# Performance work log

Measured on AMD Instinct MI355X. Metric: run time of the kernel, lower is better.

Reference implementation:

```python
import jax, jax.numpy as jnp
import numpy as np

FFT_LIST = [32, 64, 128]
C_IN = 64
C_OUT = 96
C_OUT_PER = C_OUT // len(FFT_LIST)  # 32
BASIC = FFT_LIST[1]                 # base kernel defined at fft=64 -> 33 bins
ALPHA = 0.2                         # tf.nn.leaky_relu default


def setup_inputs() -> dict:
    key = jax.random.key(0)
    k1, k2, k3, k4 = jax.random.split(key, 4)
    B, T = 8, 8192
    bins0 = BASIC // 2 + 1
    return {
        "x": jax.random.normal(k1, (B, T, C_IN), dtype=jnp.float32),
        "kernel_r": jax.random.normal(k2, (1, 1, bins0, C_IN * C_OUT_PER), dtype=jnp.float32) * 0.05,
        "kernel_i": jax.random.normal(k3, (1, 1, bins0, C_IN * C_OUT_PER), dtype=jnp.float32) * 0.05,
        "bias_r": jax.random.normal(k4, (C_OUT,), dtype=jnp.float32) * 0.05,
    }


def _resize_bins(k, bins):
    # tf.image.resize on [1, H=1, W=bins0, C]: bilinear along W, half-pixel, no antialias
    if bins == k.shape[2]:
        return k
    return jax.image.resize(k, (1, 1, bins, k.shape[3]), method="linear", antialias=False)


def _leaky(v):
    return jax.nn.leaky_relu(v, negative_slope=ALPHA)


def reference(x, kernel_r, kernel_i, bias_r):
    B, T, _ = x.shape
    xc = jnp.transpose(x, (0, 2, 1))  # [B, C_in, T]
    outs = []
    for fft_n in FFT_LIST:
        frames = T // fft_n
        bins = fft_n // 2 + 1
        # non-overlapping STFT with no window == reshape + rfft
        xf = jnp.fft.rfft(xc.reshape(B, C_IN, frames, fft_n), axis=-1)  # [B, Cin, F, K] complex64
        kr = _resize_bins(kernel_r, bins)
        ki = _resize_bins(kernel_i, bins)
        kern = (kr + 1j * ki).reshape(bins, C_IN, C_OUT_PER).astype(jnp.complex64)  # [K, Cin, Cout]
        # per-frequency-bin complex matmul over c_in (fuses tile+mul+reduce_sum)
        y = jnp.einsum("bcfk,kco->bofk", xf, kern)  # [B, Cout, F, K]
        # act_domain == 'freq': leaky relu on real and imag parts
        y = _leaky(jnp.real(y)) + 1j * _leaky(jnp.imag(y))
        # inverse STFT (step == length, no window) == irfft + reshape
        yt = jnp.fft.irfft(y, n=fft_n, axis=-1)            # [B, Cout, F, fft_n]
        yt = yt.reshape(B, C_OUT_PER, T)                    # [B, Cout, T]
        outs.append(jnp.transpose(yt, (0, 2, 1)))           # [B, T, Cout]
    out = jnp.concatenate(outs, axis=2)                     # [B, T, C_OUT]
    out = out + bias_r                                      # bias_add(real(bias))
    return out
```

## Files before the change

kernel.cpp:

```cpp
#include <hip/hip_runtime.h>
#include <stdint.h>

#define T_SZ 8192
#define NCH 96

typedef __attribute__((ext_vector_type(8))) short s8v;
typedef __attribute__((ext_vector_type(4))) float f4v;

__device__ __forceinline__ float lo_bf(uint32_t u){ return __uint_as_float(u << 16); }
__device__ __forceinline__ float hi_bf(uint32_t u){ return __uint_as_float(u & 0xffff0000u); }
__device__ __forceinline__ uint32_t f2bf(float f){
    uint32_t u = __float_as_uint(f);
    return (u + 0x7fffu + ((u >> 16) & 1u)) >> 16;
}
__device__ __forceinline__ uint32_t pk2(float a, float b){ return f2bf(a) | (f2bf(b) << 16); }

#define WS_TOTAL_PAIRS 235520
#define WD_OFF    942080
#define WD_ELEMS  27264
#define WA_OFF    996608
#define WA_ELEMS  30464
#define WD64_U16   1920
#define WD128_U16  7680
#define WA64_U16   2304
#define WA128_U16  8960
#define XF32W    4194304
#define XF64W   14680064
#define XF128W  25165824
#define Y32W    35651584
#define Y64W    41943040
#define Y128W   50331648
#define WS_WIDE 58720256

__global__ void prep_full(char* __restrict__ ws)
{
    int e = blockIdx.x * 256 + threadIdx.x;
    if (e < WD_ELEMS) {
        int N, NP, base;
        if (e < 1920)      { N = 32;  NP = 40;  base = 0; }
        else if (e < 7680) { N = 64;  NP = 72;  base = WD64_U16;  e -= 1920; }
        else               { N = 128; NP = 136; base = WD128_U16; e -= 7680; }
        int m = e / NP, t = e % NP;
        float v = 0.f;
        if (t < N && m < N + 2) {
            float ang = 6.2831853071795864769f * (float)(((m >> 1) * t) & (N - 1)) / (float)N;
            v = (m & 1) ? -sinf(ang) : cosf(ang);
        }
        ((unsigned short*)(ws + WD_OFF))[base + e] = (unsigned short)f2bf(v);
        return;
    }
    e -= WD_ELEMS;
    if (e < WA_ELEMS) {
        int N, S3, base;
        if (e < 2304)      { N = 32;  S3 = 72;  base = 0; }
        else if (e < 8960) { N = 64;  S3 = 104; base = WA64_U16;  e -= 2304; }
        else               { N = 128; S3 = 168; base = WA128_U16; e -= 8960; }
        int t = e / S3, kk = e % S3;
        int M2 = N + 2;
        float v = 0.f;
        if (kk < M2) {
            int k = kk >> 1;
            float ang = 6.2831853071795864769f * (float)((k * t) & (N - 1)) / (float)N;
            v = (kk & 1) ? -sinf(ang) : cosf(ang);
        }
        ((unsigned short*)(ws + WA_OFF))[base + e] = (unsigned short)f2bf(v);
    }
}

__global__ void prep_resize(const float* __restrict__ kr, const float* __restrict__ ki,
                            uint32_t* __restrict__ wsu)
{
    int idx = blockIdx.x * 256 + threadIdx.x;
    if (idx >= WS_TOTAL_PAIRS) return;
    int bins, rem = idx;
    if (rem < 17 * 2048)      { bins = 17; }
    else if (rem < 50 * 2048) { bins = 33; rem -= 17 * 2048; }
    else                      { bins = 65; rem -= 50 * 2048; }
    int k = rem >> 11, co = rem & 2047;
    float s  = (k + 0.5f) * (33.0f / bins) - 0.5f;
    float fl = floorf(s);
    float w1 = s - fl;
    int i0 = min(max((int)fl, 0), 32);
    int i1 = min(max((int)fl + 1, 0), 32);
    float r0 = kr[i0 * 2048 + co], r1 = kr[i1 * 2048 + co];
    float q0 = ki[i0 * 2048 + co], q1 = ki[i1 * 2048 + co];
    wsu[idx] = pk2(fmaf(w1, r1 - r0, r0), fmaf(w1, q1 - q0, q0));
}

__device__ __forceinline__ s8v ldfr(const unsigned short* p, int stride, int row0, int k0){
    int lane = threadIdx.x & 63;
    return *(const s8v*)(p + (row0 + (lane & 15)) * stride + k0 + ((lane >> 4) << 3));
}

template<int N, int NTW, int MT0, int MTN>
__device__ __forceinline__ void k1w_branch(const unsigned short* __restrict__ W,
        const unsigned short* __restrict__ xT, uint32_t* __restrict__ xfp,
        int b, int w, int nt0)
{
    constexpr int BINS = N/2+1, KS = N/32, NP = N+8;
    constexpr int F = 128/N, FRAMES = 8192/N;
    const int lane = threadIdx.x & 63;
    const int cl = lane & 15, kl = (lane >> 4) << 3, rg = (lane >> 4) * 4;

    f4v acc[MTN][NTW];
    #pragma unroll
    for (int mt = 0; mt < MTN; ++mt)
        #pragma unroll
        for (int nw = 0; nw < NTW; ++nw) { f4v zz = {0.f,0.f,0.f,0.f}; acc[mt][nw] = zz; }

    for (int ks = 0; ks < KS; ++ks) {
        s8v a[MTN];
        #pragma unroll
        for (int mt = 0; mt < MTN; ++mt) a[mt] = ldfr(W, NP, (MT0+mt)*16, ks*32);
        #pragma unroll
        for (int nw = 0; nw < NTW; ++nw) {
            int rowb = (nt0+nw)*16 + cl;
            s8v bb = *(const s8v*)(xT + (rowb & 63)*136 + (rowb >> 6)*N + ks*32 + kl);
            #pragma unroll
            for (int mt = 0; mt < MTN; ++mt)
                acc[mt][nw] = __builtin_amdgcn_mfma_f32_16x16x32_bf16(a[mt], bb, acc[mt][nw], 0, 0, 0);
        }
    }
    #pragma unroll
    for (int mt = 0; mt < MTN; ++mt)
      #pragma unroll
      for (int nw = 0; nw < NTW; ++nw) {
        int col = (nt0+nw)*16 + cl, f = col >> 6, c = col & 63;
        size_t bf = (size_t)b*FRAMES + w*F + f;
        #pragma unroll
        for (int r = 0; r < 4; r += 2) {
            int m = (MT0+mt)*16 + rg + r, k = m >> 1;
            if (k < BINS)
                xfp[((size_t)k*(8*FRAMES) + bf)*64 + c] = pk2(acc[mt][nw][r], acc[mt][nw][r+1]);
        }
      }
}

__global__ __launch_bounds__(512, 4) void k1w(const float* __restrict__ x, char* __restrict__ ws)
{
    __shared__ __align__(16) char smem[71936];
    unsigned short* xT   = (unsigned short*)smem;
    unsigned short* Wall = xT + 64*136;
    const unsigned short* WD = (const unsigned short*)(ws + WD_OFF);
    const int tid = threadIdx.x, bid = blockIdx.x;
    const int b = bid >> 6, w = bid & 63;

    for (int e = tid; e < WD_ELEMS/8; e += 512)
        *(uint4*)(Wall + e*8) = *(const uint4*)(WD + e*8);

    const float* xb = x + ((size_t)b*T_SZ + (size_t)w*128) * 64;
    {
        int e = tid;
        int c4 = e & 15, t0 = (e >> 4) * 4;
        const float* p = xb + (size_t)t0*64 + c4*4;
        float4 v0 = *(const float4*)(p);
        float4 v1 = *(const float4*)(p + 64);
        float4 v2 = *(const float4*)(p + 128);
        float4 v3 = *(const float4*)(p + 192);
        unsigned short* d = xT + (c4*4)*136 + t0;
        *(uint2*)(d)       = make_uint2(pk2(v0.x, v1.x), pk2(v2.x, v3.x));
        *(uint2*)(d + 136) = make_uint2(pk2(v0.y, v1.y), pk2(v2.y, v3.y));
        *(uint2*)(d + 272) = make_uint2(pk2(v0.z, v1.z), pk2(v2.z, v3.z));
        *(uint2*)(d + 408) = make_uint2(pk2(v0.w, v1.w), pk2(v2.w, v3.w));
    }
    __syncthreads();

    const int wv = tid >> 6;
    k1w_branch<32, 2, 0, 3>(Wall,             xT, (uint32_t*)(ws + XF32W),  b, w, wv*2);
    k1w_branch<64, 1, 0, 5>(Wall + WD64_U16,  xT, (uint32_t*)(ws + XF64W),  b, w, wv);
    if (wv < 4)
        k1w_branch<128, 1, 0, 5>(Wall + WD128_U16, xT, (uint32_t*)(ws + XF128W), b, w, wv);
    else
        k1w_branch<128, 1, 5, 4>(Wall + WD128_U16, xT, (uint32_t*)(ws + XF128W), b, w, wv & 3);
}

template<int N>
__device__ __forceinline__ void k2_body(int kbin, int mblk, char* smem,
        const float* __restrict__ kr, const float* __restrict__ ki,
        const uint32_t* __restrict__ xfp, uint32_t* __restrict__ y2p)
{
    constexpr int BINS = N/2+1, FRAMES = 8192/N, BF = 8*FRAMES;
    unsigned short* A  = (unsigned short*)smem;
    unsigned short* W2 = A + 128*136;
    const int tid = threadIdx.x;
    const int bf0 = mblk * 128;

    for (int e = tid; e < 2048; e += 256)
        *(uint4*)(A + (e>>4)*136 + (e&15)*8) =
            *((const uint4*)(xfp + ((size_t)kbin*BF + bf0 + (e>>4))*64) + (e & 15));

    {
        float s  = (kbin + 0.5f) * (33.0f / BINS) - 0.5f;
        float fl = floorf(s);
        float w1 = s - fl;
        int i0 = min(max((int)fl, 0), 32);
        int i1 = min(max((int)fl + 1, 0), 32);
        float wk = (kbin == 0 || kbin == BINS-1) ? (1.0f/N) : (2.0f/N);
        for (int e = tid; e < 2048; e += 256) {
            float r0 = kr[i0*2048 + e], r1 = kr[i1*2048 + e];
            float q0 = ki[i0*2048 + e], q1 = ki[i1*2048 + e];
            float vr = fmaf(w1, r1 - r0, r0) * wk;
            float vi = fmaf(w1, q1 - q0, q0) * wk;
            int c = e >> 5, o = e & 31;
            W2[o*136 + 2*c]          = (unsigned short)f2bf(vr);
            W2[o*136 + 2*c + 1]      = (unsigned short)f2bf(-vi);
            W2[(32+o)*136 + 2*c]     = (unsigned short)f2bf(vi);
            W2[(32+o)*136 + 2*c + 1] = (unsigned short)f2bf(vr);
        }
    }
    __syncthreads();

    const int wv = tid >> 6, lane = tid & 63;
    const int mt0 = wv * 2;
    f4v acc[2][4];
    #pragma unroll
    for (int mt = 0; mt < 2; ++mt)
        #pragma unroll
        for (int nt = 0; nt < 4; ++nt) { f4v zz = {0.f,0.f,0.f,0.f}; acc[mt][nt] = zz; }

    for (int ks = 0; ks < 4; ++ks) {
        s8v a0 = ldfr(A, 136, mt0*16, ks*32);
        s8v a1 = ldfr(A, 136, mt0*16 + 16, ks*32);
        #pragma unroll
        for (int nt = 0; nt < 4; ++nt) {
            s8v bb = ldfr(W2, 136, nt*16, ks*32);
            acc[0][nt] = __builtin_amdgcn_mfma_f32_16x16x32_bf16(a0, bb, acc[0][nt], 0, 0, 0);
            acc[1][nt] = __builtin_amdgcn_mfma_f32_16x16x32_bf16(a1, bb, acc[1][nt], 0, 0, 0);
        }
    }
    const int cl = lane & 15, rg = (lane >> 4) * 4;
    #pragma unroll
    for (int mt = 0; mt < 2; ++mt)
      #pragma unroll
      for (int nt = 0; nt < 2; ++nt) {
        int o = nt*16 + cl;
        #pragma unroll
        for (int r = 0; r < 4; ++r) {
            int bf = bf0 + (mt0+mt)*16 + rg + r;
            float re = acc[mt][nt][r];   re = (re > 0.f) ? re : 0.2f * re;
            float im = acc[mt][nt+2][r]; im = (im > 0.f) ? im : 0.2f * im;
            y2p[((size_t)bf*BINS + kbin)*32 + o] = pk2(re, im);
        }
      }
}

__global__ __launch_bounds__(256, 3) void k2all(const float* __restrict__ kr,
        const float* __restrict__ ki, char* __restrict__ ws)
{
    __shared__ __align__(16) char smem[52224];
    int bid = blockIdx.x;
    if (bid < 272)
        k2_body<32>(bid >> 4, bid & 15, smem, kr, ki,
                    (const uint32_t*)(ws + XF32W), (uint32_t*)(ws + Y32W));
    else if (bid < 536) {
        int q = bid - 272;
        k2_body<64>(q >> 3, q & 7, smem, kr, ki,
                    (const uint32_t*)(ws + XF64W), (uint32_t*)(ws + Y64W));
    } else {
        int q = bid - 536;
        k2_body<128>(q >> 2, q & 3, smem, kr, ki,
                     (const uint32_t*)(ws + XF128W), (uint32_t*)(ws + Y128W));
    }
}

template<int N, int TROWS>
__device__ __forceinline__ void k3_body(int b, int f0, int t0, char* smem,
        const unsigned short* __restrict__ WA, const uint32_t* __restrict__ y2p,
        const float* __restrict__ bias, float* __restrict__ out)
{
    constexpr int BINS = N/2+1, FRAMES = 8192/N, M2 = 2*BINS;
    constexpr int KP = ((M2+31)/32)*32, S3 = KP+8, KS = KP/32;
    constexpr int FB = (N==32)?8:(N==64)?4:2;
    constexpr int NCOLS = FB*32;
    constexpr int COFF = (N==32)?0:(N==64)?32:64;
    constexpr int NTW = (N==128)?4:8;

    unsigned short* A  = (unsigned short*)smem;
    unsigned short* Bt = A + TROWS*S3;
    const int tid = threadIdx.x;

    for (int e = tid; e < TROWS*S3/8; e += 256)
        *(uint4*)(A + e*8) = *(const uint4*)(WA + t0*S3 + e*8);

    for (int e = tid; e < FB*BINS*32; e += 256) {
        int o = e & 31, k = (e >> 5) % BINS, f = e / (32*BINS);
        size_t bf = (size_t)b*FRAMES + f0 + f;
        uint32_t v = y2p[(bf*BINS + k)*32 + o];
        *(uint32_t*)(Bt + (f*32 + o)*S3 + 2*k) = v;
    }
    for (int e = tid; e < NCOLS*15; e += 256) {
        int row = e / 15, j = e % 15;
        *(uint32_t*)(Bt + row*S3 + M2 + 2*j) = 0u;
    }
    __syncthreads();

    const int wv = tid >> 6, lane = tid & 63;
    const int mt0 = (N==32) ? (wv & 1) : wv;
    const int nt0 = (N==32) ? (wv >> 1)*8 : 0;

    f4v acc[NTW];
    #pragma unroll
    for (int nw = 0; nw < NTW; ++nw) { f4v zz = {0.f,0.f,0.f,0.f}; acc[nw] = zz; }

    for (int ks = 0; ks < KS; ++ks) {
        s8v a = ldfr(A, S3, mt0*16, ks*32);
        #pragma unroll
        for (int nw = 0; nw < NTW; ++nw) {
            s8v bb = ldfr(Bt, S3, (nt0+nw)*16, ks*32);
            acc[nw] = __builtin_amdgcn_mfma_f32_16x16x32_bf16(a, bb, acc[nw], 0, 0, 0);
        }
    }
    const int cl = lane & 15, rg = (lane >> 4) * 4;
    #pragma unroll
    for (int nw = 0; nw < NTW; ++nw) {
        int col = (nt0+nw)*16 + cl, f = col >> 5, o = col & 31;
        float bv = bias[COFF + o];
        #pragma unroll
        for (int r = 0; r < 4; ++r) {
            int t = t0 + mt0*16 + rg + r;
            out[((size_t)(b*T_SZ + (f0+f)*N + t))*NCH + COFF + o] = acc[nw][r] + bv;
        }
    }
}

__global__ __launch_bounds__(256, 3) void k3all(char* __restrict__ ws,
        const float* __restrict__ bias, float* __restrict__ out)
{
    __shared__ __align__(16) char smem[43008];
    const unsigned short* WA = (const unsigned short*)(ws + WA_OFF);
    int bid = blockIdx.x;
    if (bid < 256)
        k3_body<32,32>(bid >> 5, (bid & 31)*8, 0, smem, WA,
                       (const uint32_t*)(ws + Y32W), bias, out);
    else if (bid < 512) {
        int q = bid - 256;
        k3_body<64,64>(q >> 5, (q & 31)*4, 0, smem, WA + WA64_U16,
                       (const uint32_t*)(ws + Y64W), bias, out);
    } else {
        int q = bid - 512;
        k3_body<128,64>(q >> 6, ((q & 63) >> 1)*2, (q & 1)*64, smem, WA + WA128_U16,
                        (const uint32_t*)(ws + Y128W), bias, out);
    }
}

template<int FFT_N, bool USE_WS>
__global__ __launch_bounds__(256, 2)
void stft_fused(const float* __restrict__ x, const float* __restrict__ kr,
                const float* __restrict__ ki, const float* __restrict__ bias,
                const uint32_t* __restrict__ wsu, float* __restrict__ out)
{
    constexpr int CIN = 64, COUT = 32;
    constexpr int BINS = FFT_N / 2 + 1;
    constexpr int NFR  = 128 / FFT_N;
    constexpr int KQ   = (BINS + 3) / 4;
    constexpr int COFF = (FFT_N == 32) ? 0 : (FFT_N == 64) ? 32 : 64;
    constexpr int WSP  = (FFT_N == 32) ? 0 : (FFT_N == 64) ? 17 * 2048 : 50 * 2048;
    constexpr int XSP  = 68;
    constexpr int CP   = 66;
    constexpr int YP   = BINS + 2;
    constexpr int SMEMF = 128 * XSP + 2 * FFT_N + NFR * BINS * CP * 2;

    __shared__ __align__(16) float smem[SMEMF];
    float*  xs  = smem;
    float2* cst = (float2*)(smem + 128 * XSP);
    float2* xf2 = (float2*)(smem + 128 * XSP + 2 * FFT_N);
    float2* Y2  = (float2*)smem;

    const int tid = threadIdx.x;
    const int bid = blockIdx.x;
    const int b = bid >> 6, w = bid & 63;
    const float* xblk = x + (size_t)(b * T_SZ + w * 128) * CIN;

    for (int i = tid; i < 2048; i += 256) {
        float4 v = ((const float4*)xblk)[i];
        int t = i >> 4;
        int c = (i & 15) * 4;
        *(float4*)&xs[t * XSP + c] = v;
    }
    if (tid < FFT_N) {
        float ang = 6.2831853071795864769f * ((float)tid / (float)FFT_N);
        float sv, cv;
        sincosf(ang, &sv, &cv);
        cst[tid] = make_float2(cv, sv);
    }
    __syncthreads();

    constexpr int NT_DFT = NFR * KQ * 16;
    for (int tile = tid; tile < NT_DFT; tile += 256) {
        int cq  = tile & 15;
        int kqf = tile >> 4;
        int kq  = kqf % KQ, f = kqf / KQ;
        int k0  = kq * 4;
        float accr[4][4] = {};
        float acci[4][4] = {};
        int idx[4] = {0, 0, 0, 0};
        const float* xrow = xs + f * FFT_N * XSP + cq * 4;
        for (int t = 0; t < FFT_N; ++t) {
            float4 xv = *(const float4*)(xrow + t * XSP);
            float xc[4] = {xv.x, xv.y, xv.z, xv.w};
            #pragma unroll
            for (int kk = 0; kk < 4; ++kk) {
                float2 tw = cst[idx[kk]];
                idx[kk] = (idx[kk] + k0 + kk) & (FFT_N - 1);
                #pragma unroll
                for (int cc = 0; cc < 4; ++cc) {
                    accr[kk][cc] = fmaf(xc[cc], tw.x, accr[kk][cc]);
                    acci[kk][cc] = fmaf(xc[cc], tw.y, acci[kk][cc]);
                }
            }
        }
        #pragma unroll
        for (int kk = 0; kk < 4; ++kk) {
            int k = k0 + kk;
            if (k < BINS) {
                #pragma unroll
                for (int cc = 0; cc < 4; ++cc)
                    xf2[(f * BINS + k) * CP + cq * 4 + cc] =
                        make_float2(accr[kk][cc], -acci[kk][cc]);
            }
        }
    }
    __syncthreads();

    constexpr int NT_MM = BINS * 8;
    for (int task = tid; task < NT_MM; task += 256) {
        int oq = task & 7, k = task >> 3;
        float2 accY[NFR][4] = {};
        float w1 = 0.f; int i0 = 0, i1 = 0;
        if (!USE_WS) {
            float s  = (k + 0.5f) * (33.0f / BINS) - 0.5f;
            float fl = floorf(s); w1 = s - fl;
            i0 = min(max((int)fl, 0), 32);
            i1 = min(max((int)fl + 1, 0), 32);
        }
        const uint32_t* wp = USE_WS ? (wsu + WSP + k * 2048 + oq * 4) : (const uint32_t*)nullptr;
        for (int c = 0; c < CIN; ++c) {
            float krv[4], kiv[4];
            if (USE_WS) {
                uint4 u = *(const uint4*)(wp + c * 32);
                krv[0] = lo_bf(u.x); kiv[0] = hi_bf(u.x);
                krv[1] = lo_bf(u.y); kiv[1] = hi_bf(u.y);
                krv[2] = lo_bf(u.z); kiv[2] = hi_bf(u.z);
                krv[3] = lo_bf(u.w); kiv[3] = hi_bf(u.w);
            } else {
                const float* p = kr + (size_t)i0 * 2048 + c * 32 + oq * 4;
                const float* q = kr + (size_t)i1 * 2048 + c * 32 + oq * 4;
                float4 r0 = *(const float4*)p, r1 = *(const float4*)q;
                p = ki + (size_t)i0 * 2048 + c * 32 + oq * 4;
                q = ki + (size_t)i1 * 2048 + c * 32 + oq * 4;
                float4 q0 = *(const float4*)p, q1 = *(const float4*)q;
                krv[0] = fmaf(w1, r1.x - r0.x, r0.x); kiv[0] = fmaf(w1, q1.x - q0.x, q0.x);
                krv[1] = fmaf(w1, r1.y - r0.y, r0.y); kiv[1] = fmaf(w1, q1.y - q0.y, q0.y);
                krv[2] = fmaf(w1, r1.z - r0.z, r0.z); kiv[2] = fmaf(w1, q1.z - q0.z, q0.z);
                krv[3] = fmaf(w1, r1.w - r0.w, r0.w); kiv[3] = fmaf(w1, q1.w - q0.w, q0.w);
            }
            #pragma unroll
            for (int f = 0; f < NFR; ++f) {
                float2 xv = xf2[(f * BINS + k) * CP + c];
                #pragma unroll
                for (int jo = 0; jo < 4; ++jo) {
                    accY[f][jo].x += xv.x * krv[jo] - xv.y * kiv[jo];
                    accY[f][jo].y += xv.x * kiv[jo] + xv.y * krv[jo];
                }
            }
        }
        float wk = (k == 0 || k == BINS - 1) ? (1.0f / FFT_N) : (2.0f / FFT_N);
        #pragma unroll
        for (int f = 0; f < NFR; ++f) {
            #pragma unroll
            for (int jo = 0; jo < 4; ++jo) {
                float yr = accY[f][jo].x; yr = (yr > 0.f) ? yr : 0.2f * yr;
                float yi = accY[f][jo].y; yi = (yi > 0.f) ? yi : 0.2f * yi;
                Y2[(f * COUT + oq * 4 + jo) * YP + k] = make_float2(yr * wk, yi * wk);
            }
        }
    }
    __syncthreads();

    {
        int tq = tid >> 3, oq = tid & 7;
        int tg0 = tq * 4;
        int f   = tg0 / FFT_N;
        int tl0 = tg0 % FFT_N;
        float acc[4][4] = {};
        int idx[4] = {0, 0, 0, 0};
        const float2* yb = Y2 + (f * COUT + oq * 4) * YP;
        for (int k = 0; k < BINS; ++k) {
            float2 tw[4];
            #pragma unroll
            for (int j = 0; j < 4; ++j) {
                tw[j] = cst[idx[j]];
                idx[j] = (idx[j] + tl0 + j) & (FFT_N - 1);
            }
            #pragma unroll
            for (int jo = 0; jo < 4; ++jo) {
                float2 yv = yb[jo * YP + k];
                #pragma unroll
                for (int j = 0; j < 4; ++j)
                    acc[j][jo] += yv.x * tw[j].x - yv.y * tw[j].y;
            }
        }
        float4 bv = *(const float4*)(bias + COFF + oq * 4);
        float* ob = out + ((size_t)(b * T_SZ + w * 128 + tg0)) * NCH + COFF + oq * 4;
        #pragma unroll
        for (int j = 0; j < 4; ++j) {
            float4 o4 = make_float4(acc[j][0] + bv.x, acc[j][1] + bv.y,
                                    acc[j][2] + bv.z, acc[j][3] + bv.w);
            *(float4*)(ob + (size_t)j * NCH) = o4;
        }
    }
}

extern "C" void kernel_launch(void* const* d_in, const int* in_sizes, int n_in,
                              void* d_out, int out_size, void* d_ws, size_t ws_size,
                              hipStream_t stream)
{
    (void)in_sizes; (void)n_in; (void)out_size;
    const float* x    = (const float*)d_in[0];
    const float* kr   = (const float*)d_in[1];
    const float* ki   = (const float*)d_in[2];
    const float* bias = (const float*)d_in[3];
    float* out = (float*)d_out;
    char* ws = (char*)d_ws;
    dim3 blk(256);

    if (ws != nullptr && ws_size >= (size_t)WS_WIDE) {
        prep_full<<<dim3(226), blk, 0, stream>>>(ws);
        k1w   <<<dim3(512),  dim3(512), 0, stream>>>(x, ws);
        k2all <<<dim3(796),  blk, 0, stream>>>(kr, ki, ws);
        k3all <<<dim3(1024), blk, 0, stream>>>(ws, bias, out);
    } else if (ws != nullptr && ws_size >= (size_t)WS_TOTAL_PAIRS * 4) {
        uint32_t* wsu = (uint32_t*)ws;
        prep_resize<<<dim3(920), blk, 0, stream>>>(kr, ki, wsu);
        stft_fused<32,  true><<<dim3(512), blk, 0, stream>>>(x, kr, ki, bias, wsu, out);
        stft_fused<64,  true><<<dim3(512), blk, 0, stream>>>(x, kr, ki, bias, wsu, out);
        stft_fused<128, true><<<dim3(512), blk, 0, stream>>>(x, kr, ki, bias, wsu, out);
    } else {
        stft_fused<32,  false><<<dim3(512), blk, 0, stream>>>(x, kr, ki, bias, nullptr, out);
        stft_fused<64,  false><<<dim3(512), blk, 0, stream>>>(x, kr, ki, bias, nullptr, out);
        stft_fused<128, false><<<dim3(512), blk, 0, stream>>>(x, kr, ki, bias, nullptr, out);
    }
}
```

Measured before the change: 48.13 us.

## Generate DFT twiddle matrices in-kernel and drop the prep_full launch

The separate prep kernel that wrote bf16 DFT/IDFT matrices to workspace is removed. k1w and k3 now build those matrices in shared memory from a small sincos table computed per block, which saves one kernel launch and the global round trip. The N=128 path in k3 is retiled into smaller 32-row tiles, so the grid grows from 1024 to 1536 blocks, with a tighter smem stride and a higher occupancy hint. The cost is redundant per-block table and matrix generation, with integer div/mod work done before the matmuls.

Result: slower. 68.21 us (+41.7%).

```diff
diff --git a/kernel.cpp b/kernel.cpp
--- a/kernel.cpp
+++ b/kernel.cpp
@@ -16,14 +16,9 @@
 __device__ __forceinline__ uint32_t pk2(float a, float b){ return f2bf(a) | (f2bf(b) << 16); }
 
 #define WS_TOTAL_PAIRS 235520
-#define WD_OFF    942080
-#define WD_ELEMS  27264
-#define WA_OFF    996608
-#define WA_ELEMS  30464
 #define WD64_U16   1920
 #define WD128_U16  7680
-#define WA64_U16   2304
-#define WA128_U16  8960
+#define WD_ELEMS  27264
 #define XF32W    4194304
 #define XF64W   14680064
 #define XF128W  25165824
@@ -32,61 +27,6 @@
 #define Y128W   50331648
 #define WS_WIDE 58720256
 
-__global__ void prep_full(char* __restrict__ ws)
-{
-    int e = blockIdx.x * 256 + threadIdx.x;
-    if (e < WD_ELEMS) {
-        int N, NP, base;
-        if (e < 1920)      { N = 32;  NP = 40;  base = 0; }
-        else if (e < 7680) { N = 64;  NP = 72;  base = WD64_U16;  e -= 1920; }
-        else               { N = 128; NP = 136; base = WD128_U16; e -= 7680; }
-        int m = e / NP, t = e % NP;
-        float v = 0.f;
-        if (t < N && m < N + 2) {
-            float ang = 6.2831853071795864769f * (float)(((m >> 1) * t) & (N - 1)) / (float)N;
-            v = (m & 1) ? -sinf(ang) : cosf(ang);
-        }
-        ((unsigned short*)(ws + WD_OFF))[base + e] = (unsigned short)f2bf(v);
-        return;
-    }
-    e -= WD_ELEMS;
-    if (e < WA_ELEMS) {
-        int N, S3, base;
-        if (e < 2304)      { N = 32;  S3 = 72;  base = 0; }
-        else if (e < 8960) { N = 64;  S3 = 104; base = WA64_U16;  e -= 2304; }
-        else               { N = 128; S3 = 168; base = WA128_U16; e -= 8960; }
-        int t = e / S3, kk = e % S3;
-        int M2 = N + 2;
-        float v = 0.f;
-        if (kk < M2) {
-            int k = kk >> 1;
-            float ang = 6.2831853071795864769f * (float)((k * t) & (N - 1)) / (float)N;
-            v = (kk & 1) ? -sinf(ang) : cosf(ang);
-        }
-        ((unsigned short*)(ws + WA_OFF))[base + e] = (unsigned short)f2bf(v);
-    }
-}
-
-__global__ void prep_resize(const float* __restrict__ kr, const float* __restrict__ ki,
-                            uint32_t* __restrict__ wsu)
-{
-    int idx = blockIdx.x * 256 + threadIdx.x;
-    if (idx >= WS_TOTAL_PAIRS) return;
-    int bins, rem = idx;
-    if (rem < 17 * 2048)      { bins = 17; }
-    else if (rem < 50 * 2048) { bins = 33; rem -= 17 * 2048; }
-    else                      { bins = 65; rem -= 50 * 2048; }
-    int k = rem >> 11, co = rem & 2047;
-    float s  = (k + 0.5f) * (33.0f / bins) - 0.5f;
-    float fl = floorf(s);
-    float w1 = s - fl;
-    int i0 = min(max((int)fl, 0), 32);
-    int i1 = min(max((int)fl + 1, 0), 32);
-    float r0 = kr[i0 * 2048 + co], r1 = kr[i1 * 2048 + co];
-    float q0 = ki[i0 * 2048 + co], q1 = ki[i1 * 2048 + co];
-    wsu[idx] = pk2(fmaf(w1, r1 - r0, r0), fmaf(w1, q1 - q0, q0));
-}
-
 __device__ __forceinline__ s8v ldfr(const unsigned short* p, int stride, int row0, int k0){
     int lane = threadIdx.x & 63;
     return *(const s8v*)(p + (row0 + (lane & 15)) * stride + k0 + ((lane >> 4) << 3));
@@ -138,15 +78,33 @@
 
 __global__ __launch_bounds__(512, 4) void k1w(const float* __restrict__ x, char* __restrict__ ws)
 {
-    __shared__ __align__(16) char smem[71936];
+    __shared__ __align__(16) char smem[72960];
     unsigned short* xT   = (unsigned short*)smem;
     unsigned short* Wall = xT + 64*136;
-    const unsigned short* WD = (const unsigned short*)(ws + WD_OFF);
+    float2*         cst  = (float2*)(Wall + WD_ELEMS);
     const int tid = threadIdx.x, bid = blockIdx.x;
     const int b = bid >> 6, w = bid & 63;
 
-    for (int e = tid; e < WD_ELEMS/8; e += 512)
-        *(uint4*)(Wall + e*8) = *(const uint4*)(WD + e*8);
+    if (tid < 128) {
+        float sv, cv;
+        sincosf(6.2831853071795864769f * (float)tid / 128.0f, &sv, &cv);
+        cst[tid] = make_float2(cv, sv);
+    }
+    __syncthreads();
+
+    for (int e = tid; e < WD_ELEMS; e += 512) {
+        int N, NP, mul, e2 = e;
+        if (e2 < 1920)      { N = 32;  NP = 40;  mul = 4; }
+        else if (e2 < 7680) { N = 64;  NP = 72;  mul = 2; e2 -= 1920; }
+        else                { N = 128; NP = 136; mul = 1; e2 -= 7680; }
+        int m = e2 / NP, t = e2 % NP;
+        float v = 0.f;
+        if (t < N && m < N + 2) {
+            float2 cs = cst[(((m >> 1) * t) & (N - 1)) * mul];
+            v = (m & 1) ? -cs.y : cs.x;
+        }
+        Wall[e] = (unsigned short)f2bf(v);
+    }
 
     const float* xb = x + ((size_t)b*T_SZ + (size_t)w*128) * 64;
     {
@@ -263,30 +221,42 @@
     }
 }
 
-template<int N, int TROWS>
+template<int N, int TROWS, int NTW>
 __device__ __forceinline__ void k3_body(int b, int f0, int t0, char* smem,
-        const unsigned short* __restrict__ WA, const uint32_t* __restrict__ y2p,
-        const float* __restrict__ bias, float* __restrict__ out)
+        const uint32_t* __restrict__ y2p, const float* __restrict__ bias,
+        float* __restrict__ out)
 {
     constexpr int BINS = N/2+1, FRAMES = 8192/N, M2 = 2*BINS;
-    constexpr int KP = ((M2+31)/32)*32, S3 = KP+8, KS = KP/32;
+    constexpr int KP = ((M2+31)/32)*32, S3 = KP+4, KS = KP/32;
     constexpr int FB = (N==32)?8:(N==64)?4:2;
     constexpr int NCOLS = FB*32;
     constexpr int COFF = (N==32)?0:(N==64)?32:64;
-    constexpr int NTW = (N==128)?4:8;
-
-    unsigned short* A  = (unsigned short*)smem;
-    unsigned short* Bt = A + TROWS*S3;
+
+    float2*         cst = (float2*)smem;
+    unsigned short* A   = (unsigned short*)(smem + 1024);
+    unsigned short* Bt  = A + TROWS*S3;
     const int tid = threadIdx.x;
 
-    for (int e = tid; e < TROWS*S3/8; e += 256)
-        *(uint4*)(A + e*8) = *(const uint4*)(WA + t0*S3 + e*8);
-
+    if (tid < N) {
+        float sv, cv;
+        sincosf(6.2831853071795864769f * (float)tid / (float)N, &sv, &cv);
+        cst[tid] = make_float2(cv, sv);
+    }
+    __syncthreads();
+
+    for (int e = tid; e < TROWS*S3; e += 256) {
+        int t = e / S3, kk = e % S3;
+        float v = 0.f;
+        if (kk < M2) {
+            float2 cs = cst[((kk >> 1) * (t0 + t)) & (N - 1)];
+            v = (kk & 1) ? -cs.y : cs.x;
+        }
+        A[e] = (unsigned short)f2bf(v);
+    }
     for (int e = tid; e < FB*BINS*32; e += 256) {
         int o = e & 31, k = (e >> 5) % BINS, f = e / (32*BINS);
         size_t bf = (size_t)b*FRAMES + f0 + f;
-        uint32_t v = y2p[(bf*BINS + k)*32 + o];
-        *(uint32_t*)(Bt + (f*32 + o)*S3 + 2*k) = v;
+        *(uint32_t*)(Bt + (f*32 + o)*S3 + 2*k) = y2p[(bf*BINS + k)*32 + o];
     }
     for (int e = tid; e < NCOLS*15; e += 256) {
         int row = e / 15, j = e % 15;
@@ -295,8 +265,8 @@
     __syncthreads();
 
     const int wv = tid >> 6, lane = tid & 63;
-    const int mt0 = (N==32) ? (wv & 1) : wv;
-    const int nt0 = (N==32) ? (wv >> 1)*8 : 0;
+    const int mt0 = (N==64) ? wv : (wv & 1);
+    const int nt0 = (N==32) ? (wv >> 1)*8 : (N==64) ? 0 : (wv >> 1)*2;
 
     f4v acc[NTW];
     #pragma unroll
@@ -323,24 +293,43 @@
     }
 }
 
-__global__ __launch_bounds__(256, 3) void k3all(char* __restrict__ ws,
+__global__ __launch_bounds__(256, 4) void k3all(char* __restrict__ ws,
         const float* __restrict__ bias, float* __restrict__ out)
 {
-    __shared__ __align__(16) char smem[43008];
-    const unsigned short* WA = (const unsigned short*)(ws + WA_OFF);
+    __shared__ __align__(16) char smem[40192];
     int bid = blockIdx.x;
     if (bid < 256)
-        k3_body<32,32>(bid >> 5, (bid & 31)*8, 0, smem, WA,
-                       (const uint32_t*)(ws + Y32W), bias, out);
+        k3_body<32,32,8>(bid >> 5, (bid & 31)*8, 0, smem,
+                         (const uint32_t*)(ws + Y32W), bias, out);
     else if (bid < 512) {
         int q = bid - 256;
-        k3_body<64,64>(q >> 5, (q & 31)*4, 0, smem, WA + WA64_U16,
-                       (const uint32_t*)(ws + Y64W), bias, out);
+        k3_body<64,64,8>(q >> 5, (q & 31)*4, 0, smem,
+                         (const uint32_t*)(ws + Y64W), bias, out);
     } else {
         int q = bid - 512;
-        k3_body<128,64>(q >> 6, ((q & 63) >> 1)*2, (q & 1)*64, smem, WA + WA128_U16,
-                        (const uint32_t*)(ws + Y128W), bias, out);
-    }
+        k3_body<128,32,2>(q >> 7, ((q & 127) >> 2)*2, (q & 3)*32, smem,
+                          (const uint32_t*)(ws + Y128W), bias, out);
+    }
+}
+
+__global__ void prep_resize(const float* __restrict__ kr, const float* __restrict__ ki,
+                            uint32_t* __restrict__ wsu)
+{
+    int idx = blockIdx.x * 256 + threadIdx.x;
+    if (idx >= WS_TOTAL_PAIRS) return;
+    int bins, rem = idx;
+    if (rem < 17 * 2048)      { bins = 17; }
+    else if (rem < 50 * 2048) { bins = 33; rem -= 17 * 2048; }
+    else                      { bins = 65; rem -= 50 * 2048; }
+    int k = rem >> 11, co = rem & 2047;
+    float s  = (k + 0.5f) * (33.0f / bins) - 0.5f;
+    float fl = floorf(s);
+    float w1 = s - fl;
+    int i0 = min(max((int)fl, 0), 32);
+    int i1 = min(max((int)fl + 1, 0), 32);
+    float r0 = kr[i0 * 2048 + co], r1 = kr[i1 * 2048 + co];
+    float q0 = ki[i0 * 2048 + co], q1 = ki[i1 * 2048 + co];
+    wsu[idx] = pk2(fmaf(w1, r1 - r0, r0), fmaf(w1, q1 - q0, q0));
 }
 
 template<int FFT_N, bool USE_WS>
@@ -525,10 +514,9 @@
     dim3 blk(256);
 
     if (ws != nullptr && ws_size >= (size_t)WS_WIDE) {
-        prep_full<<<dim3(226), blk, 0, stream>>>(ws);
         k1w   <<<dim3(512),  dim3(512), 0, stream>>>(x, ws);
         k2all <<<dim3(796),  blk, 0, stream>>>(kr, ki, ws);
-        k3all <<<dim3(1024), blk, 0, stream>>>(ws, bias, out);
+        k3all <<<dim3(1536), blk, 0, stream>>>(ws, bias, out);
     } else if (ws != nullptr && ws_size >= (size_t)WS_TOTAL_PAIRS * 4) {
         uint32_t* wsu = (uint32_t*)ws;
         prep_resize<<<dim3(920), blk, 0, stream>>>(kr, ki, wsu);
```
